# Kernel tuning notes

Measured on AMD Instinct MI355X. Metric: run time of the kernel, lower is better.

## Reference

```python
import jax, jax.numpy as jnp
import numpy as np

SIZE = 5
N_RADIAL = 4
EPS = 1e-5
PAD = [(3, 3)] * 3
# (scalar_in, scalar_out, vector) per Block, from features=[1,8,16,16,16,10]
DIMS = [(1, 8, 4), (8, 16, 12), (16, 16, 16), (16, 16, 16), (16, 10, 13)]


def _basis():
    # 5^3 grid of offsets, radial hat basis and angular (Cartesian) basis tensors
    o = jnp.arange(SIZE, dtype=jnp.float32) - (SIZE - 1) / 2.0
    X, Y, Z = jnp.meshgrid(o, o, o, indexing='ij')
    r = jnp.sqrt(X ** 2 + Y ** 2 + Z ** 2)
    hats = jnp.stack([jnp.clip(1.0 - jnp.abs(r - k), 0.0, None) for k in range(N_RADIAL)])  # [K,5,5,5]
    inv = jnp.where(r > 0, 1.0 / jnp.where(r > 0, r, 1.0), 0.0)
    xhat = jnp.stack([X * inv, Y * inv, Z * inv])  # [3,5,5,5], zero at origin
    mask = (r > 0).astype(jnp.float32)
    eye = jnp.eye(3, dtype=jnp.float32)
    e = np.zeros((3, 3, 3), np.float32)
    e[0, 1, 2] = e[1, 2, 0] = e[2, 0, 1] = 1.0
    e[0, 2, 1] = e[2, 1, 0] = e[1, 0, 2] = -1.0
    eps3 = jnp.asarray(e)
    a0 = eye[:, :, None, None, None] * jnp.ones_like(r)                      # J=0: delta_ij
    a1 = jnp.einsum('ijl,lxyz->ijxyz', eps3, xhat)                           # J=1: eps_ijl xhat_l
    a2 = xhat[:, None] * xhat[None, :] - eye[:, :, None, None, None] / 3.0 * mask  # J=2 traceless sym
    ang = jnp.stack([a0, a1, a2])  # [3,3,3,5,5,5]
    return hats, xhat, ang


def _conv(x, K, stride):
    return jax.lax.conv_general_dilated(x, K, (stride,) * 3, PAD,
                                        dimension_numbers=('NCDHW', 'OIDHW', 'NCDHW'))


def _bn3d(x, gamma, beta):
    m = x.mean((0, 2, 3, 4), keepdims=True)
    v = x.var((0, 2, 3, 4), keepdims=True)
    xn = (x - m) * jax.lax.rsqrt(v + EPS)
    return xn * gamma[None, :, None, None, None] + beta[None, :, None, None, None]


def _block(s, w1, wA, wB, bias, gamma, beta, relu, hats, xhat, ang):
    vec, s_in = w1.shape[0], w1.shape[1]
    s_out = wA.shape[0]
    # conv1: scalar -> vector, equivariant kernel K1[o*3+j, i] = xhat_j * sum_k w1[o,i,k] hat_k(r)
    R1 = jnp.einsum('oik,kxyz->oixyz', w1, hats)
    K1 = (xhat[None, :, None] * R1[:, None]).reshape(vec * 3, s_in, SIZE, SIZE, SIZE)
    v = _conv(s, K1, 2)  # [B, vec*3, D,H,W]
    B = v.shape[0]
    sp = v.shape[2:]
    # TensorProduct: per-channel outer product v_i v_j -> repr3x3 (9 comps)
    vr = v.reshape(B, vec, 3, *sp)
    t = (vr[:, :, :, None] * vr[:, :, None, :]).reshape(B, vec * 9, *sp)
    vt = jnp.concatenate([v, t], axis=1)
    # conv2: (repr3 ++ repr3x3) -> scalar
    RA = jnp.einsum('ovk,kxyz->ovxyz', wA, hats)
    KA = (RA[:, :, None] * xhat[None, None]).reshape(s_out, vec * 3, SIZE, SIZE, SIZE)
    RB = jnp.einsum('ovmk,kxyz->ovmxyz', wB, hats)
    KB = jnp.einsum('ovmxyz,mijxyz->ovijxyz', RB, ang).reshape(s_out, vec * 9, SIZE, SIZE, SIZE)
    K2 = jnp.concatenate([KA, KB], axis=1)
    out = _conv(vt, K2, 1)
    out = _bn3d(out, gamma, beta)  # scalar_batch_norm=True
    if relu:  # bias_relu flag
        out = jax.nn.relu(out + bias[None, :, None, None, None])
    return out


def _forward(x, params, gamma_out, beta_out):
    hats, xhat, ang = _basis()
    # bn_in, affine=False
    m = x.mean((0, 2, 3, 4), keepdims=True)
    v = x.var((0, 2, 3, 4), keepdims=True)
    s = (x - m) * jax.lax.rsqrt(v + EPS)
    n = len(params)
    for i, (w1, wA, wB, bias, gamma, beta) in enumerate(params):
        s = _block(s, w1, wA, wB, bias, gamma, beta, i < n - 1, hats, xhat, ang)
    pooled = s.mean((2, 3, 4))  # global average pool -> [B, classes]
    m = pooled.mean(0)
    v = pooled.var(0)
    return gamma_out * (pooled - m) * jax.lax.rsqrt(v + EPS) + beta_out


def setup_inputs() -> dict:
    key = jax.random.key(0)
    ks = iter(jax.random.split(key, 64))
    inp = {'x': jax.random.normal(next(ks), (32, 1, 64, 64, 64), dtype=jnp.float32)}
    for i, (si, so, ve) in enumerate(DIMS):
        inp[f'w1_{i}'] = jax.random.normal(next(ks), (ve, si, N_RADIAL), dtype=jnp.float32) * (si * 125) ** -0.5
        inp[f'wA_{i}'] = jax.random.normal(next(ks), (so, ve, N_RADIAL), dtype=jnp.float32) * (ve * 3 * 125) ** -0.5
        inp[f'wB_{i}'] = jax.random.normal(next(ks), (so, ve, 3, N_RADIAL), dtype=jnp.float32) * (ve * 9 * 125) ** -0.5
        inp[f'bias_{i}'] = jnp.zeros((so,), jnp.float32)
        inp[f'gamma_{i}'] = jnp.ones((so,), jnp.float32)
        inp[f'beta_{i}'] = jnp.zeros((so,), jnp.float32)
    inp['gamma_out'] = jnp.ones((10,), jnp.float32)
    inp['beta_out'] = jnp.zeros((10,), jnp.float32)
    return inp


def reference(x, w1_0, wA_0, wB_0, bias_0, gamma_0, beta_0,
              w1_1, wA_1, wB_1, bias_1, gamma_1, beta_1,
              w1_2, wA_2, wB_2, bias_2, gamma_2, beta_2,
              w1_3, wA_3, wB_3, bias_3, gamma_3, beta_3,
              w1_4, wA_4, wB_4, bias_4, gamma_4, beta_4,
              gamma_out, beta_out):
    params = [
        (w1_0, wA_0, wB_0, bias_0, gamma_0, beta_0),
        (w1_1, wA_1, wB_1, bias_1, gamma_1, beta_1),
        (w1_2, wA_2, wB_2, bias_2, gamma_2, beta_2),
        (w1_3, wA_3, wB_3, bias_3, gamma_3, beta_3),
        (w1_4, wA_4, wB_4, bias_4, gamma_4, beta_4),
    ]
    return _forward(x, params, gamma_out, beta_out)
```

## Files before the change

### kernel.cpp

```cpp
#include <hip/hip_runtime.h>
#include <math.h>

#define EPSF 1e-5f

typedef _Float16 f16;
typedef __attribute__((ext_vector_type(8))) _Float16 f16x8;
typedef __attribute__((ext_vector_type(4))) float f32x4;

__device__ __forceinline__ void tap_geom(int tap, float hats[4], float xh[3], float& mask) {
  int d = tap / 25, h = (tap / 5) % 5, w = tap % 5;
  float X = (float)(d - 2), Y = (float)(h - 2), Z = (float)(w - 2);
  float r = sqrtf(X * X + Y * Y + Z * Z);
#pragma unroll
  for (int k = 0; k < 4; ++k) hats[k] = fmaxf(1.0f - fabsf(r - (float)k), 0.0f);
  float inv = (r > 0.0f) ? (1.0f / r) : 0.0f;
  xh[0] = X * inv; xh[1] = Y * inv; xh[2] = Z * inv;
  mask = (r > 0.0f) ? 1.0f : 0.0f;
}

__global__ void build_k1(const float* __restrict__ w1, float* __restrict__ K1,
                         int VEC, int SIN) {
  int total = SIN * 125 * VEC;
  for (int idx = blockIdx.x * blockDim.x + threadIdx.x; idx < total;
       idx += gridDim.x * blockDim.x) {
    int cv = idx % VEC;
    int tap = (idx / VEC) % 125;
    int i = idx / (VEC * 125);
    float hats[4], xh[3], mask;
    tap_geom(tap, hats, xh, mask);
    float R = 0.f;
#pragma unroll
    for (int k = 0; k < 4; ++k) R += w1[(cv * SIN + i) * 4 + k] * hats[k];
    float* o = K1 + (long)idx * 4;
    o[0] = xh[0] * R; o[1] = xh[1] * R; o[2] = xh[2] * R; o[3] = 0.f;
  }
}

__global__ void build_k2c(const float* __restrict__ wA, const float* __restrict__ wB,
                          f16* __restrict__ K2, int VEC, int SOUT, int KS) {
  int total = 125 * KS * 64 * 8;
  for (int idx = blockIdx.x * blockDim.x + threadIdx.x; idx < total;
       idx += gridDim.x * blockDim.x) {
    int e = idx & 7;
    int lane = (idx >> 3) & 63;
    int ks = (idx >> 9) % KS;
    int tap = idx / (KS << 9);
    int n = lane & 15;
    int g = lane >> 4;
    int c = (ks * 4 + g) * 8 + e;
    float val = 0.f;
    if (n < SOUT && c < VEC * 12) {
      float hats[4], xh[3], mask;
      tap_geom(tap, hats, xh, mask);
      int cv = c / 12, comp = c % 12;
      if (comp < 3) {
        float RA = 0.f;
#pragma unroll
        for (int k = 0; k < 4; ++k) RA += wA[(n * VEC + cv) * 4 + k] * hats[k];
        val = RA * xh[comp];
      } else {
        int ij = comp - 3;
        int ii = ij / 3, jj = ij % 3;
        float RB[3];
#pragma unroll
        for (int m = 0; m < 3; ++m) {
          float r = 0.f;
#pragma unroll
          for (int k = 0; k < 4; ++k) r += wB[((n * VEC + cv) * 3 + m) * 4 + k] * hats[k];
          RB[m] = r;
        }
        float a0 = (ii == jj) ? 1.0f : 0.0f;
        float a1 = 0.0f;
        if (ii != jj) {
          int l = 3 - ii - jj;
          float sgn = (((jj - ii + 3) % 3) == 1) ? 1.0f : -1.0f;
          a1 = sgn * xh[l];
        }
        float a2 = xh[ii] * xh[jj] - ((ii == jj) ? (mask / 3.0f) : 0.0f);
        val = RB[0] * a0 + RB[1] * a1 + RB[2] * a2;
      }
    }
    K2[idx] = (f16)val;
  }
}

template <int SIN, int VEC, int CP8>
__global__ __launch_bounds__(256) void conv1_vt_x(const float* __restrict__ s,
                                                  const f32x4* __restrict__ K1,
                                                  f16* __restrict__ VT,
                                                  int Bc, int IS, int OS, int XG) {
  constexpr int NP = (VEC + 1) / 2;
  int iss = IS * IS * IS;
  long total = (long)Bc * OS * OS * XG * NP;
  for (long idx = blockIdx.x * (long)blockDim.x + threadIdx.x; idx < total;
       idx += gridDim.x * (long)blockDim.x) {
    int xg = (int)(idx % XG);
    int pp = (int)((idx / XG) % NP);
    int y  = (int)((idx / ((long)XG * NP)) % OS);
    int z  = (int)((idx / ((long)XG * NP * OS)) % OS);
    int b  = (int)(idx / ((long)XG * NP * OS * OS));
    int x0 = xg * 4;
    int cv0 = 2 * pp;
    int cv1 = (2 * pp + 1 < VEC) ? (2 * pp + 1) : (VEC - 1);

    float acc[2][3][4];
#pragma unroll
    for (int p = 0; p < 2; ++p)
#pragma unroll
      for (int c = 0; c < 3; ++c)
#pragma unroll
        for (int t = 0; t < 4; ++t) acc[p][c][t] = 0.f;

    const float* sb = s + (long)b * SIN * iss;
    const f32x4* kb = K1;
    for (int i = 0; i < SIN; ++i) {
      for (int d = 0; d < 5; ++d) {
        int iz = 2 * z - 3 + d;
        if ((unsigned)iz >= (unsigned)IS) continue;
        for (int h = 0; h < 5; ++h) {
          int iy = 2 * y - 3 + h;
          if ((unsigned)iy >= (unsigned)IS) continue;
          const float* srow = sb + (iz * IS + iy) * IS;
          float sv[11];
#pragma unroll
          for (int m = 0; m < 11; ++m) {
            int xi = 2 * x0 - 3 + m;
            bool ok = (unsigned)xi < (unsigned)IS;
            sv[m] = ok ? srow[ok ? xi : 0] : 0.f;
          }
          const f32x4* krow = kb + (d * 25 + h * 5) * VEC;
#pragma unroll
          for (int w = 0; w < 5; ++w) {
            f32x4 k0 = krow[w * VEC + cv0];
            f32x4 k1 = krow[w * VEC + cv1];
#pragma unroll
            for (int t = 0; t < 4; ++t) {
              float sx = sv[2 * t + w];
              acc[0][0][t] = fmaf(sx, k0[0], acc[0][0][t]);
              acc[0][1][t] = fmaf(sx, k0[1], acc[0][1][t]);
              acc[0][2][t] = fmaf(sx, k0[2], acc[0][2][t]);
              acc[1][0][t] = fmaf(sx, k1[0], acc[1][0][t]);
              acc[1][1][t] = fmaf(sx, k1[1], acc[1][1][t]);
              acc[1][2][t] = fmaf(sx, k1[2], acc[1][2][t]);
            }
          }
        }
      }
      sb += iss;
      kb += 125 * VEC;
    }

    long ybase = (((long)(b * OS + z) * OS + y) * CP8) * (long)OS * 8;
    int cg0 = pp * 3;
#pragma unroll
    for (int t = 0; t < 4; ++t) {
      int x = x0 + t;
      if (x >= OS) continue;
      float a00 = acc[0][0][t], a01 = acc[0][1][t], a02 = acc[0][2][t];
      float a10 = acc[1][0][t], a11 = acc[1][1][t], a12 = acc[1][2][t];
      float v0[12] = {a00, a01, a02,
                      a00 * a00, a00 * a01, a00 * a02,
                      a01 * a00, a01 * a01, a01 * a02,
                      a02 * a00, a02 * a01, a02 * a02};
      float v1[12] = {a10, a11, a12,
                      a10 * a10, a10 * a11, a10 * a12,
                      a11 * a10, a11 * a11, a11 * a12,
                      a12 * a10, a12 * a11, a12 * a12};
      f16x8 pk0, pk1, pk2;
#pragma unroll
      for (int e = 0; e < 8; ++e) pk0[e] = (f16)v0[e];
#pragma unroll
      for (int e = 0; e < 4; ++e) { pk1[e] = (f16)v0[8 + e]; pk1[4 + e] = (f16)v1[e]; }
#pragma unroll
      for (int e = 0; e < 8; ++e) pk2[e] = (f16)v1[4 + e];
      long rowbase = ybase + (long)x * 8;
      *(f16x8*)(VT + rowbase + (long)(cg0 + 0) * OS * 8) = pk0;
      *(f16x8*)(VT + rowbase + (long)(cg0 + 1) * OS * 8) = pk1;
      *(f16x8*)(VT + rowbase + (long)(cg0 + 2) * OS * 8) = pk2;
    }
  }
}

template <int CP8, int SOUT, int ZT>
__global__ __launch_bounds__(256) void conv2_mfma(const f16* __restrict__ VT,
                                                  const f16* __restrict__ K2,
                                                  float* __restrict__ out,
                                                  int Bc, int IS, int OS, int XG, int ZG) {
  constexpr int KS = CP8 / 4;
  constexpr int NU = ZT + 4;
  int nwg = gridDim.x;
  int orig = blockIdx.x;
  int q = nwg >> 3, r = nwg & 7;
  int xcd = orig & 7, sub = orig >> 3;
  int swz = (xcd < r ? xcd * (q + 1) : r * (q + 1) + (xcd - r) * q) + sub;
  int wid = swz * (blockDim.x >> 6) + ((int)threadIdx.x >> 6);
  int lane = threadIdx.x & 63;
  int total = Bc * ZG * OS * XG;
  if (wid >= total) return;
  int xg = wid % XG;
  int y  = (wid / XG) % OS;
  int zg = (wid / (XG * OS)) % ZG;
  int b  = wid / (XG * OS * ZG);
  int z0 = zg * ZT;
  int x0 = xg * 16;
  int lm = lane & 15;
  int g  = lane >> 4;

  f32x4 acc[ZT];
#pragma unroll
  for (int t = 0; t < ZT; ++t) acc[t] = (f32x4){0.f, 0.f, 0.f, 0.f};

  const f16* kl = K2 + ((long)lane << 3);

  for (int h = 0; h < 5; ++h) {
    int yi = y - 3 + h;
    if ((unsigned)yi >= (unsigned)IS) continue;
    const f16* base[NU];
    bool zok[NU];
#pragma unroll
    for (int u = 0; u < NU; ++u) {
      int zi = z0 - 3 + u;
      zok[u] = (unsigned)zi < (unsigned)IS;
      int zc = zok[u] ? zi : 0;
      base[u] = VT + (((long)(b * IS + zc) * IS + yi) * CP8) * (long)IS * 8;
    }
    int hw = h * 5;
#pragma unroll 1
    for (int w = 0; w < 5; ++w) {
      int xi = x0 + lm - 3 + w;
      bool xok = (unsigned)xi < (unsigned)IS;
#pragma unroll
      for (int ks = 0; ks < KS; ++ks) {
        f16x8 bf[5];
#pragma unroll
        for (int d = 0; d < 5; ++d)
          bf[d] = *(const f16x8*)(kl + ((long)((d * 25 + hw + w) * KS + ks) << 9));
        f16x8 af[NU];
#pragma unroll
        for (int u = 0; u < NU; ++u) {
          af[u] = (f16x8){};
          if (zok[u] && xok)
            af[u] = *(const f16x8*)(base[u] + ((ks * 4 + g) * IS + xi) * 8);
        }
#pragma unroll
        for (int u = 0; u < NU; ++u) {
#pragma unroll
          for (int t = 0; t < ZT; ++t) {
            int d = u - t;
            if (d >= 0 && d <= 4)
              acc[t] = __builtin_amdgcn_mfma_f32_16x16x32_f16(af[u], bf[d], acc[t], 0, 0, 0);
          }
        }
      }
    }
  }
  if (lm < SOUT) {
    int oss = OS * OS * OS;
#pragma unroll
    for (int t = 0; t < ZT; ++t) {
      int z = z0 + t;
      if (z < OS) {
        float* op = out + ((long)b * SOUT + lm) * oss + (z * OS + y) * OS;
#pragma unroll
        for (int r2 = 0; r2 < 4; ++r2) {
          int xm = x0 + g * 4 + r2;
          if (xm < OS) op[xm] = acc[t][r2];
        }
      }
    }
  }
}

__global__ void stats1(const float* __restrict__ a, float* __restrict__ part,
                       int B, int C, int ss, int nblk) {
  int c = blockIdx.y;
  int tid = threadIdx.x;
  float s = 0.f, s2 = 0.f;
  for (int b = 0; b < B; ++b) {
    const float* ab = a + ((long)b * C + c) * ss;
    for (int p = blockIdx.x * blockDim.x + tid; p < ss; p += nblk * blockDim.x) {
      float x = ab[p];
      s += x;
      s2 += x * x;
    }
  }
  __shared__ float sh[256], sh2[256];
  sh[tid] = s; sh2[tid] = s2;
  __syncthreads();
  for (int off = 128; off > 0; off >>= 1) {
    if (tid < off) { sh[tid] += sh[tid + off]; sh2[tid] += sh2[tid + off]; }
    __syncthreads();
  }
  if (tid == 0) {
    part[(c * nblk + blockIdx.x) * 2 + 0] = sh[0];
    part[(c * nblk + blockIdx.x) * 2 + 1] = sh2[0];
  }
}

__global__ void stats2(const float* __restrict__ part, float* __restrict__ stats,
                       int nblk, float invn) {
  int c = blockIdx.x;
  int tid = threadIdx.x;
  float s = 0.f, s2 = 0.f;
  for (int i = tid; i < nblk; i += blockDim.x) {
    s += part[(c * nblk + i) * 2 + 0];
    s2 += part[(c * nblk + i) * 2 + 1];
  }
  __shared__ float sh[256], sh2[256];
  sh[tid] = s; sh2[tid] = s2;
  __syncthreads();
  for (int off = 128; off > 0; off >>= 1) {
    if (tid < off) { sh[tid] += sh[tid + off]; sh2[tid] += sh2[tid + off]; }
    __syncthreads();
  }
  if (tid == 0) {
    float m = sh[0] * invn;
    float var = sh2[0] * invn - m * m;
    stats[c * 2 + 0] = m;
    stats[c * 2 + 1] = 1.0f / sqrtf(var + EPSF);
  }
}

__global__ void bn_apply(const float* __restrict__ in, float* __restrict__ out,
                         const float* __restrict__ stats, const float* __restrict__ g,
                         const float* __restrict__ be, const float* __restrict__ bias,
                         int C, int ss, int relu) {
  int bc = blockIdx.y;
  int c = bc % C;
  float m = stats[c * 2 + 0];
  float r = stats[c * 2 + 1];
  float ga = g ? g[c] : 1.f;
  float bb = be ? be[c] : 0.f;
  float bi = bias ? bias[c] : 0.f;
  const float* ip = in + (long)bc * ss;
  float* op = out + (long)bc * ss;
  for (int p = blockIdx.x * blockDim.x + threadIdx.x; p < ss; p += gridDim.x * blockDim.x) {
    float xn = (ip[p] - m) * r * ga + bb;
    if (relu) xn = fmaxf(xn + bi, 0.f);
    op[p] = xn;
  }
}

__global__ void pool_k(const float* __restrict__ in, float* __restrict__ pooled, int ss) {
  int bc = blockIdx.x;
  int tid = threadIdx.x;
  const float* p = in + (long)bc * ss;
  float s = 0.f;
  for (int e = tid; e < ss; e += blockDim.x) s += p[e];
  __shared__ float sh[256];
  sh[tid] = s;
  __syncthreads();
  for (int off = 128; off > 0; off >>= 1) {
    if (tid < off) sh[tid] += sh[tid + off];
    __syncthreads();
  }
  if (tid == 0) pooled[bc] = sh[0] / (float)ss;
}

__global__ void final_bn(const float* __restrict__ pooled, const float* __restrict__ g,
                         const float* __restrict__ be, float* __restrict__ out,
                         int B, int C) {
  int tid = threadIdx.x;
  __shared__ float mv[16][2];
  if (tid < C) {
    float s = 0.f, s2 = 0.f;
    for (int b = 0; b < B; ++b) {
      float x = pooled[b * C + tid];
      s += x;
      s2 += x * x;
    }
    float m = s / (float)B;
    float var = s2 / (float)B - m * m;
    mv[tid][0] = m;
    mv[tid][1] = 1.0f / sqrtf(var + EPSF);
  }
  __syncthreads();
  for (int i = tid; i < B * C; i += blockDim.x) {
    int c = i % C;
    out[i] = g[c] * (pooled[i] - mv[c][0]) * mv[c][1] + be[c];
  }
}

extern "C" void kernel_launch(void* const* d_in, const int* in_sizes, int n_in,
                              void* d_out, int out_size, void* d_ws, size_t ws_size,
                              hipStream_t stream) {
  (void)in_sizes; (void)n_in; (void)out_size; (void)ws_size;
  const float* x = (const float*)d_in[0];
  const float* w1[5]; const float* wA[5]; const float* wB[5];
  const float* bias[5]; const float* gam[5]; const float* bet[5];
  for (int i = 0; i < 5; ++i) {
    w1[i]  = (const float*)d_in[1 + i * 6 + 0];
    wA[i]  = (const float*)d_in[1 + i * 6 + 1];
    wB[i]  = (const float*)d_in[1 + i * 6 + 2];
    bias[i]= (const float*)d_in[1 + i * 6 + 3];
    gam[i] = (const float*)d_in[1 + i * 6 + 4];
    bet[i] = (const float*)d_in[1 + i * 6 + 5];
  }
  const float* gamma_out = (const float*)d_in[31];
  const float* beta_out  = (const float*)d_in[32];
  float* out = (float*)d_out;

  float* A     = (float*)d_ws;
  float* Bb    = A + 8388608;
  float* V     = Bb + 10976000;
  float* K1    = V + 13799808;
  float* K2    = K1 + 128000;
  float* part  = K2 + 384000;
  float* stats = part + 16 * 256 * 2;
  float* pooled= stats + 64;
  f16* VT  = (f16*)V;
  f16* K2h = (f16*)K2;

  const int NB = 256;
  const int Bn = 32;
  const int ZT = 4;

  {
    int ss = 64 * 64 * 64;
    stats1<<<dim3(NB, 1), 256, 0, stream>>>(x, part, Bn, 1, ss, NB);
    stats2<<<1, 256, 0, stream>>>(part, stats, NB, 1.0f / (float)(Bn * (long)ss));
    int gx = (ss + 255) / 256;
    bn_apply<<<dim3(gx, Bn), 256, 0, stream>>>(x, A, stats, nullptr, nullptr, nullptr, 1, ss, 0);
  }

  const int SINs[5]  = {1, 8, 16, 16, 16};
  const int SOUTs[5] = {8, 16, 16, 16, 10};
  const int VECs[5]  = {4, 12, 16, 16, 13};
  const int ISs[5]   = {64, 35, 21, 14, 10};
  const int VSs[5]   = {33, 19, 12, 8, 6};
  const int OSs[5]   = {35, 21, 14, 10, 8};
  const int CP8s[5]  = {8, 24, 24, 24, 24};
  const int CHKs[5]  = {8, 16, 32, 32, 32};
  const int NPs[5]   = {2, 6, 8, 8, 7};

  float* sbuf = A;
  for (int i = 0; i < 5; ++i) {
    float* obuf = (i % 2 == 0) ? Bb : A;
    int IS = ISs[i], VS = VSs[i], OS = OSs[i];
    int VEC = VECs[i], SIN = SINs[i], SOUT = SOUTs[i];

    { int t = SIN * 125 * VEC;
      build_k1<<<(t + 255) / 256, 256, 0, stream>>>(w1[i], K1, VEC, SIN); }

    int CP8 = CP8s[i];
    int KS = CP8 / 4;
    int CHK = CHKs[i];
    int XG = (OS + 15) / 16;
    int ZG = (OS + ZT - 1) / ZT;
    int XG1 = (VS + 3) / 4;
    { int t = 125 * KS * 512;
      build_k2c<<<(t + 255) / 256, 256, 0, stream>>>(wA[i], wB[i], K2h, VEC, SOUT, KS); }
    for (int b0 = 0; b0 < Bn; b0 += CHK) {
      int bc = CHK;
      const float* sp = sbuf + (long)b0 * SIN * IS * IS * IS;
      float* op = obuf + (long)b0 * SOUT * OS * OS * OS;
      long t1 = (long)bc * VS * VS * XG1 * NPs[i];
      int g1 = (int)((t1 + 255) / 256);
      long waves = (long)bc * ZG * OS * XG;
      int g2 = (int)((waves * 64 + 255) / 256);
      switch (i) {
        case 0:
          conv1_vt_x<1, 4, 8><<<g1, 256, 0, stream>>>(sp, (const f32x4*)K1, VT, bc, IS, VS, XG1);
          conv2_mfma<8, 8, ZT><<<g2, 256, 0, stream>>>(VT, K2h, op, bc, VS, OS, XG, ZG);
          break;
        case 1:
          conv1_vt_x<8, 12, 24><<<g1, 256, 0, stream>>>(sp, (const f32x4*)K1, VT, bc, IS, VS, XG1);
          conv2_mfma<24, 16, ZT><<<g2, 256, 0, stream>>>(VT, K2h, op, bc, VS, OS, XG, ZG);
          break;
        case 2:
          conv1_vt_x<16, 16, 24><<<g1, 256, 0, stream>>>(sp, (const f32x4*)K1, VT, bc, IS, VS, XG1);
          conv2_mfma<24, 16, ZT><<<g2, 256, 0, stream>>>(VT, K2h, op, bc, VS, OS, XG, ZG);
          break;
        case 3:
          conv1_vt_x<16, 16, 24><<<g1, 256, 0, stream>>>(sp, (const f32x4*)K1, VT, bc, IS, VS, XG1);
          conv2_mfma<24, 16, ZT><<<g2, 256, 0, stream>>>(VT, K2h, op, bc, VS, OS, XG, ZG);
          break;
        case 4:
          conv1_vt_x<16, 13, 24><<<g1, 256, 0, stream>>>(sp, (const f32x4*)K1, VT, bc, IS, VS, XG1);
          conv2_mfma<24, 10, ZT><<<g2, 256, 0, stream>>>(VT, K2h, op, bc, VS, OS, XG, ZG);
          break;
      }
    }

    { int ss = OS * OS * OS;
      stats1<<<dim3(NB, SOUT), 256, 0, stream>>>(obuf, part, Bn, SOUT, ss, NB);
      stats2<<<SOUT, 256, 0, stream>>>(part, stats, NB, 1.0f / (float)((long)Bn * ss));
      int gx = (ss + 255) / 256;
      bn_apply<<<dim3(gx, Bn * SOUT), 256, 0, stream>>>(obuf, obuf, stats, gam[i], bet[i],
                                                        bias[i], SOUT, ss, (i < 4) ? 1 : 0);
    }
    sbuf = obuf;
  }

  pool_k<<<Bn * 10, 256, 0, stream>>>(sbuf, pooled, 8 * 8 * 8);
  final_bn<<<1, 64, 0, stream>>>(pooled, gamma_out, beta_out, out, Bn, 10);
}
```

Before: 3.621 ms.

## Split conv1 input channels into slices with separate reduce-and-pack kernel for late layers

```diff
diff --git a/kernel.cpp b/kernel.cpp
--- a/kernel.cpp
+++ b/kernel.cpp
@@ -178,6 +178,141 @@
       *(f16x8*)(VT + rowbase + (long)(cg0 + 1) * OS * 8) = pk1;
       *(f16x8*)(VT + rowbase + (long)(cg0 + 2) * OS * 8) = pk2;
     }
+  }
+}
+
+template <int SIN, int NSL, int VEC>
+__global__ __launch_bounds__(256) void conv1_part(const float* __restrict__ s,
+                                                  const f32x4* __restrict__ K1,
+                                                  float* __restrict__ Vp,
+                                                  int Bc, int IS, int OS, int XG, int XP) {
+  constexpr int NP = (VEC + 1) / 2;
+  constexpr int SLC = SIN / NSL;
+  constexpr int V3 = VEC * 3;
+  int iss = IS * IS * IS;
+  long total = (long)Bc * OS * OS * NP * NSL * XG;
+  for (long idx = blockIdx.x * (long)blockDim.x + threadIdx.x; idx < total;
+       idx += gridDim.x * (long)blockDim.x) {
+    int xg = (int)(idx % XG);
+    int sl = (int)((idx / XG) % NSL);
+    int pp = (int)((idx / ((long)XG * NSL)) % NP);
+    int y  = (int)((idx / ((long)XG * NSL * NP)) % OS);
+    int z  = (int)((idx / ((long)XG * NSL * NP * OS)) % OS);
+    int b  = (int)(idx / ((long)XG * NSL * NP * OS * OS));
+    int x0 = xg * 4;
+    int cv0 = 2 * pp;
+    int cv1 = (2 * pp + 1 < VEC) ? (2 * pp + 1) : (VEC - 1);
+
+    float acc[2][3][4];
+#pragma unroll
+    for (int p = 0; p < 2; ++p)
+#pragma unroll
+      for (int c = 0; c < 3; ++c)
+#pragma unroll
+        for (int t = 0; t < 4; ++t) acc[p][c][t] = 0.f;
+
+    const float* sb = s + ((long)b * SIN + sl * SLC) * iss;
+    const f32x4* kb = K1 + (long)(sl * SLC) * 125 * VEC;
+    for (int i = 0; i < SLC; ++i) {
+      for (int d = 0; d < 5; ++d) {
+        int iz = 2 * z - 3 + d;
+        if ((unsigned)iz >= (unsigned)IS) continue;
+        for (int h = 0; h < 5; ++h) {
+          int iy = 2 * y - 3 + h;
+          if ((unsigned)iy >= (unsigned)IS) continue;
+          const float* srow = sb + (iz * IS + iy) * IS;
+          float sv[11];
+#pragma unroll
+          for (int m = 0; m < 11; ++m) {
+            int xi = 2 * x0 - 3 + m;
+            bool ok = (unsigned)xi < (unsigned)IS;
+            sv[m] = ok ? srow[ok ? xi : 0] : 0.f;
+          }
+          const f32x4* krow = kb + (d * 25 + h * 5) * VEC;
+#pragma unroll
+          for (int w = 0; w < 5; ++w) {
+            f32x4 k0 = krow[w * VEC + cv0];
+            f32x4 k1 = krow[w * VEC + cv1];
+#pragma unroll
+            for (int t = 0; t < 4; ++t) {
+              float sx = sv[2 * t + w];
+              acc[0][0][t] = fmaf(sx, k0[0], acc[0][0][t]);
+              acc[0][1][t] = fmaf(sx, k0[1], acc[0][1][t]);
+              acc[0][2][t] = fmaf(sx, k0[2], acc[0][2][t]);
+              acc[1][0][t] = fmaf(sx, k1[0], acc[1][0][t]);
+              acc[1][1][t] = fmaf(sx, k1[1], acc[1][1][t]);
+              acc[1][2][t] = fmaf(sx, k1[2], acc[1][2][t]);
+            }
+          }
+        }
+      }
+      sb += iss;
+      kb += 125 * VEC;
+    }
+
+    long row = (((long)sl * Bc + b) * OS + z) * OS + y;
+    float* base = Vp + row * V3 * XP + x0;
+#pragma unroll
+    for (int p = 0; p < 2; ++p) {
+      int cv = p ? cv1 : cv0;
+#pragma unroll
+      for (int c = 0; c < 3; ++c) {
+        f32x4 st = {acc[p][c][0], acc[p][c][1], acc[p][c][2], acc[p][c][3]};
+        *(f32x4*)(base + (long)(cv * 3 + c) * XP) = st;
+      }
+    }
+  }
+}
+
+template <int VEC, int NSL, int CP8>
+__global__ __launch_bounds__(256) void vt_pack(const float* __restrict__ Vp,
+                                               f16* __restrict__ VT,
+                                               int Bc, int OS, int XP) {
+  constexpr int NP = (VEC + 1) / 2;
+  constexpr int V3 = VEC * 3;
+  long total = (long)Bc * OS * OS * NP * OS;
+  for (long idx = blockIdx.x * (long)blockDim.x + threadIdx.x; idx < total;
+       idx += gridDim.x * (long)blockDim.x) {
+    int x  = (int)(idx % OS);
+    int pp = (int)((idx / OS) % NP);
+    int y  = (int)((idx / ((long)OS * NP)) % OS);
+    int z  = (int)((idx / ((long)OS * NP * OS)) % OS);
+    int b  = (int)(idx / ((long)OS * NP * OS * OS));
+    int cv0 = 2 * pp;
+    int cv1 = (2 * pp + 1 < VEC) ? (2 * pp + 1) : (VEC - 1);
+
+    float a[6] = {0.f, 0.f, 0.f, 0.f, 0.f, 0.f};
+    for (int sl = 0; sl < NSL; ++sl) {
+      long row = (((long)sl * Bc + b) * OS + z) * OS + y;
+      const float* base = Vp + row * V3 * XP + x;
+#pragma unroll
+      for (int c = 0; c < 3; ++c) {
+        a[c]     += base[(long)(cv0 * 3 + c) * XP];
+        a[3 + c] += base[(long)(cv1 * 3 + c) * XP];
+      }
+    }
+    float a00 = a[0], a01 = a[1], a02 = a[2];
+    float a10 = a[3], a11 = a[4], a12 = a[5];
+    float v0[12] = {a00, a01, a02,
+                    a00 * a00, a00 * a01, a00 * a02,
+                    a01 * a00, a01 * a01, a01 * a02,
+                    a02 * a00, a02 * a01, a02 * a02};
+    float v1[12] = {a10, a11, a12,
+                    a10 * a10, a10 * a11, a10 * a12,
+                    a11 * a10, a11 * a11, a11 * a12,
+                    a12 * a10, a12 * a11, a12 * a12};
+    f16x8 pk0, pk1, pk2;
+#pragma unroll
+    for (int e = 0; e < 8; ++e) pk0[e] = (f16)v0[e];
+#pragma unroll
+    for (int e = 0; e < 4; ++e) { pk1[e] = (f16)v0[8 + e]; pk1[4 + e] = (f16)v1[e]; }
+#pragma unroll
+    for (int e = 0; e < 8; ++e) pk2[e] = (f16)v1[4 + e];
+    long rowbase = (((long)(b * OS + z) * OS + y) * CP8) * (long)OS * 8 + (long)x * 8;
+    int cg0 = pp * 3;
+    *(f16x8*)(VT + rowbase + (long)(cg0 + 0) * OS * 8) = pk0;
+    *(f16x8*)(VT + rowbase + (long)(cg0 + 1) * OS * 8) = pk1;
+    *(f16x8*)(VT + rowbase + (long)(cg0 + 2) * OS * 8) = pk2;
   }
 }
 
@@ -448,37 +583,48 @@
     int XG = (OS + 15) / 16;
     int ZG = (OS + ZT - 1) / ZT;
     int XG1 = (VS + 3) / 4;
+    int XP1 = XG1 * 4;
     { int t = 125 * KS * 512;
       build_k2c<<<(t + 255) / 256, 256, 0, stream>>>(wA[i], wB[i], K2h, VEC, SOUT, KS); }
     for (int b0 = 0; b0 < Bn; b0 += CHK) {
       int bc = CHK;
       const float* sp = sbuf + (long)b0 * SIN * IS * IS * IS;
       float* op = obuf + (long)b0 * SOUT * OS * OS * OS;
-      long t1 = (long)bc * VS * VS * XG1 * NPs[i];
-      int g1 = (int)((t1 + 255) / 256);
       long waves = (long)bc * ZG * OS * XG;
       int g2 = (int)((waves * 64 + 255) / 256);
-      switch (i) {
-        case 0:
+      if (i <= 1) {
+        long t1 = (long)bc * VS * VS * XG1 * NPs[i];
+        int g1 = (int)((t1 + 255) / 256);
+        if (i == 0) {
           conv1_vt_x<1, 4, 8><<<g1, 256, 0, stream>>>(sp, (const f32x4*)K1, VT, bc, IS, VS, XG1);
           conv2_mfma<8, 8, ZT><<<g2, 256, 0, stream>>>(VT, K2h, op, bc, VS, OS, XG, ZG);
-          break;
-        case 1:
+        } else {
           conv1_vt_x<8, 12, 24><<<g1, 256, 0, stream>>>(sp, (const f32x4*)K1, VT, bc, IS, VS, XG1);
           conv2_mfma<24, 16, ZT><<<g2, 256, 0, stream>>>(VT, K2h, op, bc, VS, OS, XG, ZG);
-          break;
-        case 2:
-          conv1_vt_x<16, 16, 24><<<g1, 256, 0, stream>>>(sp, (const f32x4*)K1, VT, bc, IS, VS, XG1);
-          conv2_mfma<24, 16, ZT><<<g2, 256, 0, stream>>>(VT, K2h, op, bc, VS, OS, XG, ZG);
-          break;
-        case 3:
-          conv1_vt_x<16, 16, 24><<<g1, 256, 0, stream>>>(sp, (const f32x4*)K1, VT, bc, IS, VS, XG1);
-          conv2_mfma<24, 16, ZT><<<g2, 256, 0, stream>>>(VT, K2h, op, bc, VS, OS, XG, ZG);
-          break;
-        case 4:
-          conv1_vt_x<16, 13, 24><<<g1, 256, 0, stream>>>(sp, (const f32x4*)K1, VT, bc, IS, VS, XG1);
-          conv2_mfma<24, 10, ZT><<<g2, 256, 0, stream>>>(VT, K2h, op, bc, VS, OS, XG, ZG);
-          break;
+        }
+      } else {
+        float* Vp = obuf;
+        long tA = (long)bc * VS * VS * NPs[i] * 4 * XG1;
+        int gA = (int)((tA + 255) / 256);
+        long tB = (long)bc * VS * VS * NPs[i] * VS;
+        int gB = (int)((tB + 255) / 256);
+        switch (i) {
+          case 2:
+            conv1_part<16, 4, 16><<<gA, 256, 0, stream>>>(sp, (const f32x4*)K1, Vp, bc, IS, VS, XG1, XP1);
+            vt_pack<16, 4, 24><<<gB, 256, 0, stream>>>(Vp, VT, bc, VS, XP1);
+            conv2_mfma<24, 16, ZT><<<g2, 256, 0, stream>>>(VT, K2h, op, bc, VS, OS, XG, ZG);
+            break;
+          case 3:
+            conv1_part<16, 4, 16><<<gA, 256, 0, stream>>>(sp, (const f32x4*)K1, Vp, bc, IS, VS, XG1, XP1);
+            vt_pack<16, 4, 24><<<gB, 256, 0, stream>>>(Vp, VT, bc, VS, XP1);
+            conv2_mfma<24, 16, ZT><<<g2, 256, 0, stream>>>(VT, K2h, op, bc, VS, OS, XG, ZG);
+            break;
+          case 4:
+            conv1_part<16, 4, 13><<<gA, 256, 0, stream>>>(sp, (const f32x4*)K1, Vp, bc, IS, VS, XG1, XP1);
+            vt_pack<13, 4, 24><<<gB, 256, 0, stream>>>(Vp, VT, bc, VS, XP1);
+            conv2_mfma<24, 10, ZT><<<g2, 256, 0, stream>>>(VT, K2h, op, bc, VS, OS, XG, ZG);
+            break;
+        }
       }
     }
 
```

Result: faster. 3.521 ms (-2.8%).
